# Kernel tuning notes

Hardware: AMD Instinct MI355X
Metric: run time of the kernel (lower is better)

Reference implementation:

```python
import jax, jax.numpy as jnp
import numpy as np

CUTOFF = 4.0
RBF_N = 32          # distance_embedding_size == D_rbf
F_DIM = 128         # hidden_size
N_ATOMS = 20000
N_PROBES = 100000
N_EDGES = 262144
LN_EPS = 1e-5


def setup_inputs() -> dict:
    key = jax.random.key(0)
    ks = jax.random.split(key, 20)
    s = 0.02
    inp = {
        "diff_pi": jax.random.normal(ks[0], (N_EDGES, 3), jnp.float32),
        "S_JK": jax.random.normal(ks[1], (N_ATOMS, F_DIM), jnp.float32),
        "V_JK": jax.random.normal(ks[2], (N_ATOMS, 3, F_DIM), jnp.float32),
        "atom_idx": jax.random.randint(ks[3], (N_EDGES,), 0, N_ATOMS),
        "probe_idx": jax.random.randint(ks[4], (N_EDGES,), 0, N_PROBES),
        "num_probes": N_PROBES,
        # state branch params
        "w_s1": jax.random.normal(ks[5], (3 * F_DIM, F_DIM), jnp.float32) * s,
        "b_s1": jnp.zeros((F_DIM,), jnp.float32),
        "g_ln": jnp.ones((F_DIM,), jnp.float32),
        "b_ln": jnp.zeros((F_DIM,), jnp.float32),
        "w_s2": jax.random.normal(ks[6], (F_DIM, F_DIM), jnp.float32) * s,
        "b_s2": jnp.zeros((F_DIM,), jnp.float32),
        # filter branch params
        "w_f1": jax.random.normal(ks[7], (RBF_N, F_DIM), jnp.float32) * s,
        "b_f1": jnp.zeros((F_DIM,), jnp.float32),
        "w_f2": jax.random.normal(ks[8], (F_DIM, F_DIM), jnp.float32) * s,
        "b_f2": jnp.zeros((F_DIM,), jnp.float32),
        # output head params
        "w_o1": jax.random.normal(ks[9], (F_DIM, F_DIM // 2), jnp.float32) * s,
        "b_o1": jnp.zeros((F_DIM // 2,), jnp.float32),
        "w_o2": jax.random.normal(ks[10], (F_DIM // 2, 1), jnp.float32) * s,
        "b_o2": jnp.zeros((1,), jnp.float32),
        "final_bias": jnp.array([-6.1], jnp.float32),
    }
    return inp


def reference(diff_pi, S_JK, V_JK, atom_idx, probe_idx, num_probes,
              w_s1, b_s1, g_ln, b_ln, w_s2, b_s2,
              w_f1, b_f1, w_f2, b_f2,
              w_o1, b_o1, w_o2, b_o2, final_bias):
    silu = jax.nn.silu
    # edge distances
    sq = (diff_pi ** 2).sum(-1)                       # [E]
    dist = jnp.sqrt(sq)                               # [E] exact distance
    dist_safe = jnp.sqrt(sq + 1e-8)[:, None]          # [E,1]
    r_hat = diff_pi / dist_safe                       # [E,3]

    # sinc RBF expansion: sin(n*pi*d/cutoff)/d, n=1..RBF_N
    n = jnp.arange(1, RBF_N + 1, dtype=diff_pi.dtype) # [D]
    e_pi = jnp.sin(dist[:, None] * n * (jnp.pi / CUTOFF)) / dist[:, None]  # [E,D]

    # gather atom features to edges
    n_i = jnp.sqrt((V_JK ** 2).sum(1) + 1e-8)         # [N,F]
    n_e = n_i[atom_idx]                               # [E,F]
    V_e = V_JK[atom_idx]                              # [E,3,F]
    q_pi = (V_e * r_hat[:, :, None]).sum(1)           # [E,F]
    S_e = S_JK[atom_idx]                              # [E,F]

    # state branch: Linear -> LayerNorm -> SiLU -> Linear
    h = jnp.concatenate([S_e, n_e, q_pi], axis=-1)    # [E,3F]
    u = h @ w_s1 + b_s1                               # [E,F]
    mu = u.mean(-1, keepdims=True)
    var = ((u - mu) ** 2).mean(-1, keepdims=True)
    u_norm = (u - mu) / jnp.sqrt(var + LN_EPS) * g_ln + b_ln
    state = silu(u_norm) @ w_s2 + b_s2                # [E,F]

    # filter branch (no normalization -> absolute distance scale)
    W = silu(e_pi @ w_f1 + b_f1) @ w_f2 + b_f2        # [E,F]

    # fuse + output head
    m = (silu((W * state) @ w_o1 + b_o1) @ w_o2 + b_o2)[:, 0]  # [E]

    x = dist / CUTOFF
    env = 1.0 - 21.0 * x ** 5 + 35.0 * x ** 6 - 15.0 * x ** 7
    env = jnp.where(dist < CUTOFF, env, jnp.zeros_like(env))
    m_w = m * env

    # scatter-add to probes
    rho = jax.ops.segment_sum(m_w, probe_idx, num_segments=num_probes)
    return rho + final_bias[0]
```

## Files before the change

### kernel.cpp

```cpp
#include <hip/hip_runtime.h>

#define EPB     64
#define E_TOTAL 262144
#define NPROBE  100000
#define N_ATOMS 20000

#define ASTR   136
#define A2_O   0
#define F1_O   8704
#define EPI_O  17408
#define LDS_SH 19968

#define WS1_O  0
#define WS2_O  49152
#define WF1_O  65536
#define WF2_O  69632
#define WO1_O  86016
#define WT_TOT 94208
#define PQ_O   WT_TOT

typedef __attribute__((ext_vector_type(8))) short          short8;
typedef __attribute__((ext_vector_type(8))) unsigned short ushort8;
typedef __attribute__((ext_vector_type(4))) float          floatx4;

#define MFMA16(a, b, c) __builtin_amdgcn_mfma_f32_16x16x32_bf16((a), (b), (c), 0, 0, 0)

__device__ __forceinline__ short f2bf(float x) {
    unsigned u = __builtin_bit_cast(unsigned, x);
    u = (u + 0x7FFFu + ((u >> 16) & 1u)) >> 16;
    return (short)(unsigned short)u;
}
__device__ __forceinline__ unsigned pk2(float lo, float hi) {
    return __builtin_amdgcn_perm(__builtin_bit_cast(unsigned, hi),
                                 __builtin_bit_cast(unsigned, lo), 0x07060302u);
}
__device__ __forceinline__ float bf2f(unsigned short u) {
    return __builtin_bit_cast(float, ((unsigned)u) << 16);
}
__device__ __forceinline__ float silu_f(float x) {
    return x * __builtin_amdgcn_rcpf(1.0f + __expf(-x));
}

struct F8 { float v[8]; };
__device__ __forceinline__ F8 ld8(const float* __restrict__ p) {
    F8 r;
    const float4 a = *(const float4*)p;
    const float4 b = *(const float4*)(p + 4);
    r.v[0] = a.x; r.v[1] = a.y; r.v[2] = a.z; r.v[3] = a.w;
    r.v[4] = b.x; r.v[5] = b.y; r.v[6] = b.z; r.v[7] = b.w;
    return r;
}

__global__ void cfr_prep_w(const float* __restrict__ w_s1, const float* __restrict__ w_s2,
                           const float* __restrict__ w_f1, const float* __restrict__ w_f2,
                           const float* __restrict__ w_o1,
                           const float* __restrict__ fb, float* __restrict__ out,
                           unsigned short* __restrict__ wt) {
    int i = blockIdx.x * 256 + threadIdx.x;
    if (i < NPROBE) out[i] = fb[0];
    if (i < WT_TOT) {
        float v;
        if (i < WS2_O)      { int n = i / 384, k = i - n * 384;          v = w_s1[k * 128 + n]; }
        else if (i < WF1_O) { int j = i - WS2_O, n = j >> 7, k = j & 127; v = w_s2[k * 128 + n]; }
        else if (i < WF2_O) { int j = i - WF1_O, n = j >> 5, k = j & 31;  v = w_f1[k * 128 + n]; }
        else if (i < WO1_O) { int j = i - WF2_O, n = j >> 7, k = j & 127; v = w_f2[k * 128 + n]; }
        else                { int j = i - WO1_O, n = j >> 7, k = j & 127; v = w_o1[k * 64 + n]; }
        wt[i] = (unsigned short)f2bf(v);
    }
}

__global__ __launch_bounds__(256, 2) void cfr_prep_pq(
    const float* __restrict__ S, const float* __restrict__ V,
    const float* __restrict__ b_s1,
    const unsigned short* __restrict__ wt, unsigned short* __restrict__ pq)
{
    __shared__ __align__(16) unsigned short bufH[64 * 256];
    __shared__ __align__(16) unsigned short bufV[192 * 128];

    const int t    = threadIdx.x;
    const int a0   = blockIdx.x * 64;
    const int wave = t >> 6;
    const int lane = t & 63;
    const int q    = lane >> 4;
    const int c16  = lane & 15;

#pragma unroll
    for (int it = 0; it < 4; ++it) {
        int idx = it * 256 + t;
        int al = idx >> 4, f8 = (idx & 15) * 8;
        int a = a0 + al;
        ushort8 sS, sN, s0, s1, s2;
        if (a < N_ATOMS) {
            F8 s  = ld8(S + a * 128 + f8);
            F8 v0 = ld8(V + a * 384 + f8);
            F8 v1 = ld8(V + a * 384 + 128 + f8);
            F8 v2 = ld8(V + a * 384 + 256 + f8);
#pragma unroll
            for (int j = 0; j < 8; ++j) {
                sS[j] = (unsigned short)f2bf(s.v[j]);
                sN[j] = (unsigned short)f2bf(sqrtf(v0.v[j]*v0.v[j] + v1.v[j]*v1.v[j] + v2.v[j]*v2.v[j] + 1e-8f));
                s0[j] = (unsigned short)f2bf(v0.v[j]);
                s1[j] = (unsigned short)f2bf(v1.v[j]);
                s2[j] = (unsigned short)f2bf(v2.v[j]);
            }
        } else {
#pragma unroll
            for (int j = 0; j < 8; ++j) { sS[j]=0; sN[j]=0; s0[j]=0; s1[j]=0; s2[j]=0; }
        }
        const unsigned swH = (unsigned)((al & 7) << 4);
        char* hrow  = (char*)bufH + al * 512;
        char* vbase = (char*)bufV;
        *(ushort8*)(hrow + ((f8 * 2) ^ swH))         = sS;
        *(ushort8*)(hrow + ((256 + f8 * 2) ^ swH))   = sN;
        *(ushort8*)(vbase + al * 256         + ((f8 * 2) ^ swH)) = s0;
        *(ushort8*)(vbase + (64 + al) * 256  + ((f8 * 2) ^ swH)) = s1;
        *(ushort8*)(vbase + (128 + al) * 256 + ((f8 * 2) ^ swH)) = s2;
    }
    __syncthreads();

    const floatx4 zero4 = {0.f, 0.f, 0.f, 0.f};
    const unsigned swr = (unsigned)((c16 & 7) << 4);
    float bs1c[2];
#pragma unroll
    for (int ni = 0; ni < 2; ++ni) bs1c[ni] = b_s1[wave * 32 + ni * 16 + c16];

    {
        floatx4 pacc[4][2];
#pragma unroll
        for (int mi = 0; mi < 4; ++mi) { pacc[mi][0] = zero4; pacc[mi][1] = zero4; }
#pragma unroll
        for (int kk = 0; kk < 8; ++kk) {
            short8 bfr[2], af[4];
#pragma unroll
            for (int ni = 0; ni < 2; ++ni) {
                int n = wave * 32 + ni * 16 + c16;
                bfr[ni] = *(const short8*)&wt[WS1_O + n * 384 + kk * 32 + q * 8];
            }
#pragma unroll
            for (int mi = 0; mi < 4; ++mi) {
                int row = mi * 16 + c16;
                af[mi] = *(const short8*)((const char*)bufH + row * 512 + ((unsigned)(kk * 64 + q * 16) ^ swr));
            }
#pragma unroll
            for (int mi = 0; mi < 4; ++mi)
#pragma unroll
                for (int ni = 0; ni < 2; ++ni)
                    pacc[mi][ni] = MFMA16(af[mi], bfr[ni], pacc[mi][ni]);
        }
#pragma unroll
        for (int mi = 0; mi < 4; ++mi)
#pragma unroll
            for (int r = 0; r < 4; ++r) {
                int a = a0 + mi * 16 + q * 4 + r;
                if (a < N_ATOMS)
#pragma unroll
                    for (int ni = 0; ni < 2; ++ni) {
                        int col = wave * 32 + ni * 16 + c16;
                        pq[a * 512 + col] = (unsigned short)f2bf(pacc[mi][ni][r] + bs1c[ni]);
                    }
            }
    }

    short8 bq[4][2];
#pragma unroll
    for (int kk = 0; kk < 4; ++kk)
#pragma unroll
        for (int ni = 0; ni < 2; ++ni) {
            int n = wave * 32 + ni * 16 + c16;
            bq[kk][ni] = *(const short8*)&wt[WS1_O + n * 384 + 256 + kk * 32 + q * 8];
        }
#pragma unroll
    for (int d = 0; d < 3; ++d) {
        floatx4 qacc[4][2];
#pragma unroll
        for (int mi = 0; mi < 4; ++mi) { qacc[mi][0] = zero4; qacc[mi][1] = zero4; }
#pragma unroll
        for (int kk = 0; kk < 4; ++kk) {
            short8 af[4];
#pragma unroll
            for (int mi = 0; mi < 4; ++mi) {
                int row = d * 64 + mi * 16 + c16;
                af[mi] = *(const short8*)((const char*)bufV + row * 256 + ((unsigned)(kk * 64 + q * 16) ^ swr));
            }
#pragma unroll
            for (int mi = 0; mi < 4; ++mi)
#pragma unroll
                for (int ni = 0; ni < 2; ++ni)
                    qacc[mi][ni] = MFMA16(af[mi], bq[kk][ni], qacc[mi][ni]);
        }
#pragma unroll
        for (int mi = 0; mi < 4; ++mi)
#pragma unroll
            for (int r = 0; r < 4; ++r) {
                int a = a0 + mi * 16 + q * 4 + r;
                if (a < N_ATOMS)
#pragma unroll
                    for (int ni = 0; ni < 2; ++ni) {
                        int col = wave * 32 + ni * 16 + c16;
                        pq[a * 512 + (1 + d) * 128 + col] = (unsigned short)f2bf(qacc[mi][ni][r]);
                    }
            }
    }
}

__global__ __launch_bounds__(256, 4) void cfr_main(
    const float* __restrict__ diff,
    const int* __restrict__ atom_idx, const int* __restrict__ probe_idx,
    const unsigned short* __restrict__ wt, const unsigned short* __restrict__ pq,
    const float* __restrict__ g_ln, const float* __restrict__ b_ln,
    const float* __restrict__ b_s2, const float* __restrict__ b_f1,
    const float* __restrict__ b_f2, const float* __restrict__ b_o1,
    const float* __restrict__ w_o2, const float* __restrict__ b_o2,
    float* __restrict__ out)
{
    __shared__ __align__(16) unsigned short LDSu[LDS_SH];
    float* mpart = (float*)&LDSu[EPI_O];

    const int t    = threadIdx.x;
    const int e0   = blockIdx.x * EPB;
    const int wave = t >> 6;
    const int lane = t & 63;
    const int q    = lane >> 4;
    const int c16  = lane & 15;
    const floatx4 zero4 = {0.f, 0.f, 0.f, 0.f};

    {
        const int el = t >> 2;
        const int c0 = (t & 3) * 32;
        const int eg = e0 + el;
        const int a  = atom_idx[eg];
        float dx = diff[eg * 3 + 0], dy = diff[eg * 3 + 1], dz = diff[eg * 3 + 2];
        float sq   = dx * dx + dy * dy + dz * dz;
        float dist = sqrtf(sq);
        float rinv = rsqrtf(sq + 1e-8f);
        float rx = dx * rinv, ry = dy * rinv, rz = dz * rinv;

        const ushort8* pqr = (const ushort8*)(pq + a * 512 + c0);
        float u[32];
#pragma unroll
        for (int g = 0; g < 4; ++g) {
            ushort8 v = pqr[g];
#pragma unroll
            for (int j = 0; j < 8; ++j) u[g * 8 + j] = bf2f(v[j]);
        }
#pragma unroll
        for (int g = 0; g < 4; ++g) {
            ushort8 v = pqr[16 + g];
#pragma unroll
            for (int j = 0; j < 8; ++j) u[g * 8 + j] = fmaf(bf2f(v[j]), rx, u[g * 8 + j]);
        }
#pragma unroll
        for (int g = 0; g < 4; ++g) {
            ushort8 v = pqr[32 + g];
#pragma unroll
            for (int j = 0; j < 8; ++j) u[g * 8 + j] = fmaf(bf2f(v[j]), ry, u[g * 8 + j]);
        }
#pragma unroll
        for (int g = 0; g < 4; ++g) {
            ushort8 v = pqr[48 + g];
#pragma unroll
            for (int j = 0; j < 8; ++j) u[g * 8 + j] = fmaf(bf2f(v[j]), rz, u[g * 8 + j]);
        }
        float s = 0.f, s2 = 0.f;
#pragma unroll
        for (int j = 0; j < 32; ++j) { s += u[j]; s2 = fmaf(u[j], u[j], s2); }
        s  += __shfl_xor(s, 1);  s  += __shfl_xor(s, 2);
        s2 += __shfl_xor(s2, 1); s2 += __shfl_xor(s2, 2);
        float mu = s * (1.f / 128.f);
        float rstd = rsqrtf(s2 * (1.f / 128.f) - mu * mu + 1e-5f);
        const float4* gp = (const float4*)(g_ln + c0);
        const float4* bp = (const float4*)(b_ln + c0);
        unsigned pko[16];
#pragma unroll
        for (int g4 = 0; g4 < 8; ++g4) {
            float4 gg = gp[g4], bb = bp[g4];
            float y0 = silu_f((u[g4 * 4 + 0] - mu) * rstd * gg.x + bb.x);
            float y1 = silu_f((u[g4 * 4 + 1] - mu) * rstd * gg.y + bb.y);
            float y2 = silu_f((u[g4 * 4 + 2] - mu) * rstd * gg.z + bb.z);
            float y3 = silu_f((u[g4 * 4 + 3] - mu) * rstd * gg.w + bb.w);
            pko[g4 * 2 + 0] = pk2(y0, y1);
            pko[g4 * 2 + 1] = pk2(y2, y3);
        }
        uint4* dst = (uint4*)&LDSu[A2_O + el * ASTR + c0];
        dst[0] = make_uint4(pko[0], pko[1], pko[2], pko[3]);
        dst[1] = make_uint4(pko[4], pko[5], pko[6], pko[7]);
        dst[2] = make_uint4(pko[8], pko[9], pko[10], pko[11]);
        dst[3] = make_uint4(pko[12], pko[13], pko[14], pko[15]);
        float inv = __builtin_amdgcn_rcpf(dist);
        float d8  = dist * 0.125f;
        float sv[8];
#pragma unroll
        for (int j = 0; j < 8; ++j) {
            float nf = (float)((t & 3) * 8 + j + 1);
            sv[j] = __builtin_amdgcn_sinf(d8 * nf) * inv;
        }
        *(uint4*)&LDSu[EPI_O + el * 40 + (t & 3) * 8] =
            make_uint4(pk2(sv[0], sv[1]), pk2(sv[2], sv[3]), pk2(sv[4], sv[5]), pk2(sv[6], sv[7]));
    }
    __syncthreads();

    {
        short8 ae[4], be[2];
#pragma unroll
        for (int mi = 0; mi < 4; ++mi)
            ae[mi] = *(const short8*)&LDSu[EPI_O + (mi * 16 + c16) * 40 + q * 8];
#pragma unroll
        for (int ni = 0; ni < 2; ++ni) {
            int n = wave * 32 + ni * 16 + c16;
            be[ni] = *(const short8*)&wt[WF1_O + n * 32 + q * 8];
        }
        floatx4 facc[4][2];
#pragma unroll
        for (int mi = 0; mi < 4; ++mi)
#pragma unroll
            for (int ni = 0; ni < 2; ++ni)
                facc[mi][ni] = MFMA16(ae[mi], be[ni], zero4);
        float bf1c[2];
#pragma unroll
        for (int ni = 0; ni < 2; ++ni) bf1c[ni] = b_f1[wave * 32 + ni * 16 + c16];
#pragma unroll
        for (int mi = 0; mi < 4; ++mi)
#pragma unroll
            for (int r = 0; r < 4; ++r) {
                int row = mi * 16 + q * 4 + r;
#pragma unroll
                for (int ni = 0; ni < 2; ++ni) {
                    float v = facc[mi][ni][r] + bf1c[ni];
                    LDSu[F1_O + row * ASTR + (wave * 32 + ni * 16 + c16)] =
                        (unsigned short)(__builtin_bit_cast(unsigned, silu_f(v)) >> 16);
                }
            }
    }
    __syncthreads();

    {
        floatx4 sacc[4][2], wacc[4][2];
#pragma unroll
        for (int mi = 0; mi < 4; ++mi)
#pragma unroll
            for (int ni = 0; ni < 2; ++ni) { sacc[mi][ni] = zero4; wacc[mi][ni] = zero4; }
#pragma unroll
        for (int kk = 0; kk < 4; ++kk) {
            short8 a2f[4], f1f[4], b2[2], bw[2];
#pragma unroll
            for (int ni = 0; ni < 2; ++ni) {
                int n = wave * 32 + ni * 16 + c16;
                b2[ni] = *(const short8*)&wt[WS2_O + n * 128 + kk * 32 + q * 8];
                bw[ni] = *(const short8*)&wt[WF2_O + n * 128 + kk * 32 + q * 8];
            }
#pragma unroll
            for (int mi = 0; mi < 4; ++mi) {
                a2f[mi] = *(const short8*)&LDSu[A2_O + (mi * 16 + c16) * ASTR + kk * 32 + q * 8];
                f1f[mi] = *(const short8*)&LDSu[F1_O + (mi * 16 + c16) * ASTR + kk * 32 + q * 8];
            }
#pragma unroll
            for (int mi = 0; mi < 4; ++mi)
#pragma unroll
                for (int ni = 0; ni < 2; ++ni) {
                    sacc[mi][ni] = MFMA16(a2f[mi], b2[ni], sacc[mi][ni]);
                    wacc[mi][ni] = MFMA16(f1f[mi], bw[ni], wacc[mi][ni]);
                }
        }
        __syncthreads();
        float bs2c[2], bf2c[2];
#pragma unroll
        for (int ni = 0; ni < 2; ++ni) {
            int col = wave * 32 + ni * 16 + c16;
            bs2c[ni] = b_s2[col]; bf2c[ni] = b_f2[col];
        }
#pragma unroll
        for (int mi = 0; mi < 4; ++mi)
#pragma unroll
            for (int r = 0; r < 4; ++r) {
                int row = mi * 16 + q * 4 + r;
#pragma unroll
                for (int ni = 0; ni < 2; ++ni) {
                    float g = (sacc[mi][ni][r] + bs2c[ni]) * (wacc[mi][ni][r] + bf2c[ni]);
                    LDSu[A2_O + row * ASTR + (wave * 32 + ni * 16 + c16)] =
                        (unsigned short)(__builtin_bit_cast(unsigned, g) >> 16);
                }
            }
    }
    __syncthreads();

    {
        const int n2 = wave * 16 + c16;
        floatx4 oacc[4];
#pragma unroll
        for (int mi = 0; mi < 4; ++mi) oacc[mi] = zero4;
#pragma unroll
        for (int kk = 0; kk < 4; ++kk) {
            short8 bfr = *(const short8*)&wt[WO1_O + n2 * 128 + kk * 32 + q * 8];
#pragma unroll
            for (int mi = 0; mi < 4; ++mi) {
                short8 af = *(const short8*)&LDSu[A2_O + (mi * 16 + c16) * ASTR + kk * 32 + q * 8];
                oacc[mi] = MFMA16(af, bfr, oacc[mi]);
            }
        }
        float bo1c = b_o1[n2], wo2c = w_o2[n2];
#pragma unroll
        for (int mi = 0; mi < 4; ++mi)
#pragma unroll
            for (int r = 0; r < 4; ++r) {
                float s = silu_f(oacc[mi][r] + bo1c) * wo2c;
#pragma unroll
                for (int d = 1; d < 16; d <<= 1) s += __shfl_xor(s, d, 64);
                if (c16 == 0) mpart[(mi * 16 + q * 4 + r) * 4 + wave] = s;
            }
    }
    __syncthreads();

    if (t < EPB) {
        int eg = e0 + t;
        float m = mpart[t * 4 + 0] + mpart[t * 4 + 1] + mpart[t * 4 + 2] + mpart[t * 4 + 3] + b_o2[0];
        float dx = diff[eg * 3 + 0], dy = diff[eg * 3 + 1], dz = diff[eg * 3 + 2];
        float dist = sqrtf(dx * dx + dy * dy + dz * dz);
        float x  = dist * 0.25f;
        float x2 = x * x, x4 = x2 * x2;
        float x5 = x4 * x, x6 = x5 * x, x7 = x6 * x;
        float env = 1.0f - 21.0f * x5 + 35.0f * x6 - 15.0f * x7;
        env = (dist < 4.0f) ? env : 0.0f;
        float mw = m * env;
        if (mw != 0.f) unsafeAtomicAdd(&out[probe_idx[eg]], mw);
    }
}

extern "C" void kernel_launch(void* const* d_in, const int* in_sizes, int n_in,
                              void* d_out, int out_size, void* d_ws, size_t ws_size,
                              hipStream_t stream) {
    const float* diff    = (const float*)d_in[0];
    const float* S_JK    = (const float*)d_in[1];
    const float* V_JK    = (const float*)d_in[2];
    const int*   atom_i  = (const int*)d_in[3];
    const int*   probe_i = (const int*)d_in[4];
    const float* w_s1 = (const float*)d_in[6];
    const float* b_s1 = (const float*)d_in[7];
    const float* g_ln = (const float*)d_in[8];
    const float* b_ln = (const float*)d_in[9];
    const float* w_s2 = (const float*)d_in[10];
    const float* b_s2 = (const float*)d_in[11];
    const float* w_f1 = (const float*)d_in[12];
    const float* b_f1 = (const float*)d_in[13];
    const float* w_f2 = (const float*)d_in[14];
    const float* b_f2 = (const float*)d_in[15];
    const float* w_o1 = (const float*)d_in[16];
    const float* b_o1 = (const float*)d_in[17];
    const float* w_o2 = (const float*)d_in[18];
    const float* b_o2 = (const float*)d_in[19];
    const float* fbias = (const float*)d_in[20];
    float* out = (float*)d_out;

    unsigned short* wt = (unsigned short*)d_ws;
    unsigned short* pqp = wt + PQ_O;

    cfr_prep_w<<<(NPROBE + 255) / 256, 256, 0, stream>>>(w_s1, w_s2, w_f1, w_f2, w_o1,
                                                         fbias, out, wt);
    cfr_prep_pq<<<(N_ATOMS + 63) / 64, 256, 0, stream>>>(S_JK, V_JK, b_s1, wt, pqp);
    cfr_main<<<E_TOTAL / EPB, 256, 0, stream>>>(diff, atom_i, probe_i, wt, pqp,
        g_ln, b_ln, b_s2, b_f1, b_f2, b_o1, w_o2, b_o2, out);
}
```

Measured before the change: 232.1 us.

## Halve edges per block to 32 with two-wave blocks and wider per-wave tiles

The main kernel now handles 32 edges per block with 128 threads (2 waves) instead of 64 edges with 256 threads. Each wave covers 64 output columns instead of 32 in the MLP GEMMs, and the output head uses two column tiles per wave. The per-edge distance is cached in LDS so the final envelope step no longer reloads diff. The aim is smaller LDS use per block and more resident blocks, at the cost of more weight fragment loads per edge and more registers per wave.

```diff
diff --git a/kernel.cpp b/kernel.cpp
--- a/kernel.cpp
+++ b/kernel.cpp
@@ -1,15 +1,17 @@
 #include <hip/hip_runtime.h>
 
-#define EPB     64
+#define EPB     32
+#define THREADS 128
 #define E_TOTAL 262144
 #define NPROBE  100000
 #define N_ATOMS 20000
 
 #define ASTR   136
 #define A2_O   0
-#define F1_O   8704
-#define EPI_O  17408
-#define LDS_SH 19968
+#define F1_O   4352
+#define EPI_O  8704
+#define DIST_O 9984
+#define LDS_SH 10048
 
 #define WS1_O  0
 #define WS2_O  49152
@@ -203,7 +205,7 @@
     }
 }
 
-__global__ __launch_bounds__(256, 4) void cfr_main(
+__global__ __launch_bounds__(THREADS, 4) void cfr_main(
     const float* __restrict__ diff,
     const int* __restrict__ atom_idx, const int* __restrict__ probe_idx,
     const unsigned short* __restrict__ wt, const unsigned short* __restrict__ pq,
@@ -215,6 +217,7 @@
 {
     __shared__ __align__(16) unsigned short LDSu[LDS_SH];
     float* mpart = (float*)&LDSu[EPI_O];
+    float* distL = (float*)&LDSu[DIST_O];
 
     const int t    = threadIdx.x;
     const int e0   = blockIdx.x * EPB;
@@ -226,7 +229,8 @@
 
     {
         const int el = t >> 2;
-        const int c0 = (t & 3) * 32;
+        const int cc = t & 3;
+        const int c0 = cc * 32;
         const int eg = e0 + el;
         const int a  = atom_idx[eg];
         float dx = diff[eg * 3 + 0], dy = diff[eg * 3 + 1], dz = diff[eg * 3 + 2];
@@ -234,6 +238,7 @@
         float dist = sqrtf(sq);
         float rinv = rsqrtf(sq + 1e-8f);
         float rx = dx * rinv, ry = dy * rinv, rz = dz * rinv;
+        if (cc == 0) distL[el] = dist;
 
         const ushort8* pqr = (const ushort8*)(pq + a * 512 + c0);
         float u[32];
@@ -291,42 +296,42 @@
         float sv[8];
 #pragma unroll
         for (int j = 0; j < 8; ++j) {
-            float nf = (float)((t & 3) * 8 + j + 1);
+            float nf = (float)(cc * 8 + j + 1);
             sv[j] = __builtin_amdgcn_sinf(d8 * nf) * inv;
         }
-        *(uint4*)&LDSu[EPI_O + el * 40 + (t & 3) * 8] =
+        *(uint4*)&LDSu[EPI_O + el * 40 + cc * 8] =
             make_uint4(pk2(sv[0], sv[1]), pk2(sv[2], sv[3]), pk2(sv[4], sv[5]), pk2(sv[6], sv[7]));
     }
     __syncthreads();
 
     {
-        short8 ae[4], be[2];
-#pragma unroll
-        for (int mi = 0; mi < 4; ++mi)
+        short8 ae[2], be[4];
+#pragma unroll
+        for (int mi = 0; mi < 2; ++mi)
             ae[mi] = *(const short8*)&LDSu[EPI_O + (mi * 16 + c16) * 40 + q * 8];
 #pragma unroll
-        for (int ni = 0; ni < 2; ++ni) {
-            int n = wave * 32 + ni * 16 + c16;
+        for (int ni = 0; ni < 4; ++ni) {
+            int n = wave * 64 + ni * 16 + c16;
             be[ni] = *(const short8*)&wt[WF1_O + n * 32 + q * 8];
         }
-        floatx4 facc[4][2];
-#pragma unroll
-        for (int mi = 0; mi < 4; ++mi)
-#pragma unroll
-            for (int ni = 0; ni < 2; ++ni)
+        floatx4 facc[2][4];
+#pragma unroll
+        for (int mi = 0; mi < 2; ++mi)
+#pragma unroll
+            for (int ni = 0; ni < 4; ++ni)
                 facc[mi][ni] = MFMA16(ae[mi], be[ni], zero4);
-        float bf1c[2];
-#pragma unroll
-        for (int ni = 0; ni < 2; ++ni) bf1c[ni] = b_f1[wave * 32 + ni * 16 + c16];
-#pragma unroll
-        for (int mi = 0; mi < 4; ++mi)
+        float bf1c[4];
+#pragma unroll
+        for (int ni = 0; ni < 4; ++ni) bf1c[ni] = b_f1[wave * 64 + ni * 16 + c16];
+#pragma unroll
+        for (int mi = 0; mi < 2; ++mi)
 #pragma unroll
             for (int r = 0; r < 4; ++r) {
                 int row = mi * 16 + q * 4 + r;
 #pragma unroll
-                for (int ni = 0; ni < 2; ++ni) {
+                for (int ni = 0; ni < 4; ++ni) {
                     float v = facc[mi][ni][r] + bf1c[ni];
-                    LDSu[F1_O + row * ASTR + (wave * 32 + ni * 16 + c16)] =
+                    LDSu[F1_O + row * ASTR + (wave * 64 + ni * 16 + c16)] =
                         (unsigned short)(__builtin_bit_cast(unsigned, silu_f(v)) >> 16);
                 }
             }
@@ -334,49 +339,49 @@
     __syncthreads();
 
     {
-        floatx4 sacc[4][2], wacc[4][2];
-#pragma unroll
-        for (int mi = 0; mi < 4; ++mi)
-#pragma unroll
-            for (int ni = 0; ni < 2; ++ni) { sacc[mi][ni] = zero4; wacc[mi][ni] = zero4; }
+        floatx4 sacc[2][4], wacc[2][4];
+#pragma unroll
+        for (int mi = 0; mi < 2; ++mi)
+#pragma unroll
+            for (int ni = 0; ni < 4; ++ni) { sacc[mi][ni] = zero4; wacc[mi][ni] = zero4; }
 #pragma unroll
         for (int kk = 0; kk < 4; ++kk) {
-            short8 a2f[4], f1f[4], b2[2], bw[2];
-#pragma unroll
-            for (int ni = 0; ni < 2; ++ni) {
-                int n = wave * 32 + ni * 16 + c16;
+            short8 a2f[2], f1f[2], b2[4], bw[4];
+#pragma unroll
+            for (int ni = 0; ni < 4; ++ni) {
+                int n = wave * 64 + ni * 16 + c16;
                 b2[ni] = *(const short8*)&wt[WS2_O + n * 128 + kk * 32 + q * 8];
                 bw[ni] = *(const short8*)&wt[WF2_O + n * 128 + kk * 32 + q * 8];
             }
 #pragma unroll
-            for (int mi = 0; mi < 4; ++mi) {
+            for (int mi = 0; mi < 2; ++mi) {
                 a2f[mi] = *(const short8*)&LDSu[A2_O + (mi * 16 + c16) * ASTR + kk * 32 + q * 8];
                 f1f[mi] = *(const short8*)&LDSu[F1_O + (mi * 16 + c16) * ASTR + kk * 32 + q * 8];
             }
 #pragma unroll
-            for (int mi = 0; mi < 4; ++mi)
-#pragma unroll
-                for (int ni = 0; ni < 2; ++ni) {
+            for (int mi = 0; mi < 2; ++mi)
+#pragma unroll
+                for (int ni = 0; ni < 4; ++ni) {
                     sacc[mi][ni] = MFMA16(a2f[mi], b2[ni], sacc[mi][ni]);
                     wacc[mi][ni] = MFMA16(f1f[mi], bw[ni], wacc[mi][ni]);
                 }
         }
         __syncthreads();
-        float bs2c[2], bf2c[2];
-#pragma unroll
-        for (int ni = 0; ni < 2; ++ni) {
-            int col = wave * 32 + ni * 16 + c16;
+        float bs2c[4], bf2c[4];
+#pragma unroll
+        for (int ni = 0; ni < 4; ++ni) {
+            int col = wave * 64 + ni * 16 + c16;
             bs2c[ni] = b_s2[col]; bf2c[ni] = b_f2[col];
         }
 #pragma unroll
-        for (int mi = 0; mi < 4; ++mi)
+        for (int mi = 0; mi < 2; ++mi)
 #pragma unroll
             for (int r = 0; r < 4; ++r) {
                 int row = mi * 16 + q * 4 + r;
 #pragma unroll
-                for (int ni = 0; ni < 2; ++ni) {
+                for (int ni = 0; ni < 4; ++ni) {
                     float g = (sacc[mi][ni][r] + bs2c[ni]) * (wacc[mi][ni][r] + bf2c[ni]);
-                    LDSu[A2_O + row * ASTR + (wave * 32 + ni * 16 + c16)] =
+                    LDSu[A2_O + row * ASTR + (wave * 64 + ni * 16 + c16)] =
                         (unsigned short)(__builtin_bit_cast(unsigned, g) >> 16);
                 }
             }
@@ -384,37 +389,48 @@
     __syncthreads();
 
     {
-        const int n2 = wave * 16 + c16;
-        floatx4 oacc[4];
-#pragma unroll
-        for (int mi = 0; mi < 4; ++mi) oacc[mi] = zero4;
+        floatx4 oacc[2][2];
+#pragma unroll
+        for (int mi = 0; mi < 2; ++mi) { oacc[mi][0] = zero4; oacc[mi][1] = zero4; }
 #pragma unroll
         for (int kk = 0; kk < 4; ++kk) {
-            short8 bfr = *(const short8*)&wt[WO1_O + n2 * 128 + kk * 32 + q * 8];
-#pragma unroll
-            for (int mi = 0; mi < 4; ++mi) {
+            short8 bfr[2];
+#pragma unroll
+            for (int ni = 0; ni < 2; ++ni) {
+                int n2 = wave * 32 + ni * 16 + c16;
+                bfr[ni] = *(const short8*)&wt[WO1_O + n2 * 128 + kk * 32 + q * 8];
+            }
+#pragma unroll
+            for (int mi = 0; mi < 2; ++mi) {
                 short8 af = *(const short8*)&LDSu[A2_O + (mi * 16 + c16) * ASTR + kk * 32 + q * 8];
-                oacc[mi] = MFMA16(af, bfr, oacc[mi]);
-            }
-        }
-        float bo1c = b_o1[n2], wo2c = w_o2[n2];
-#pragma unroll
-        for (int mi = 0; mi < 4; ++mi)
+#pragma unroll
+                for (int ni = 0; ni < 2; ++ni)
+                    oacc[mi][ni] = MFMA16(af, bfr[ni], oacc[mi][ni]);
+            }
+        }
+        float bo1c[2], wo2c[2];
+#pragma unroll
+        for (int ni = 0; ni < 2; ++ni) {
+            int n2 = wave * 32 + ni * 16 + c16;
+            bo1c[ni] = b_o1[n2]; wo2c[ni] = w_o2[n2];
+        }
+#pragma unroll
+        for (int mi = 0; mi < 2; ++mi)
 #pragma unroll
             for (int r = 0; r < 4; ++r) {
-                float s = silu_f(oacc[mi][r] + bo1c) * wo2c;
+                float s = silu_f(oacc[mi][0][r] + bo1c[0]) * wo2c[0]
+                        + silu_f(oacc[mi][1][r] + bo1c[1]) * wo2c[1];
 #pragma unroll
                 for (int d = 1; d < 16; d <<= 1) s += __shfl_xor(s, d, 64);
-                if (c16 == 0) mpart[(mi * 16 + q * 4 + r) * 4 + wave] = s;
+                if (c16 == 0) mpart[(mi * 16 + q * 4 + r) * 2 + wave] = s;
             }
     }
     __syncthreads();
 
     if (t < EPB) {
         int eg = e0 + t;
-        float m = mpart[t * 4 + 0] + mpart[t * 4 + 1] + mpart[t * 4 + 2] + mpart[t * 4 + 3] + b_o2[0];
-        float dx = diff[eg * 3 + 0], dy = diff[eg * 3 + 1], dz = diff[eg * 3 + 2];
-        float dist = sqrtf(dx * dx + dy * dy + dz * dz);
+        float m = mpart[t * 2 + 0] + mpart[t * 2 + 1] + b_o2[0];
+        float dist = distL[t];
         float x  = dist * 0.25f;
         float x2 = x * x, x4 = x2 * x2;
         float x5 = x4 * x, x6 = x5 * x, x7 = x6 * x;
@@ -456,6 +472,6 @@
     cfr_prep_w<<<(NPROBE + 255) / 256, 256, 0, stream>>>(w_s1, w_s2, w_f1, w_f2, w_o1,
                                                          fbias, out, wt);
     cfr_prep_pq<<<(N_ATOMS + 63) / 64, 256, 0, stream>>>(S_JK, V_JK, b_s1, wt, pqp);
-    cfr_main<<<E_TOTAL / EPB, 256, 0, stream>>>(diff, atom_i, probe_i, wt, pqp,
+    cfr_main<<<E_TOTAL / EPB, THREADS, 0, stream>>>(diff, atom_i, probe_i, wt, pqp,
         g_ln, b_ln, b_s2, b_f1, b_f2, b_o1, w_o2, b_o2, out);
 }
```

Result: slower. 265.9 us (+14.6%).

## Counting-sort edges by atom index before main kernel to improve gather locality

Applied to the files above, without the earlier changes.

Adds histogram, single-block scan, and scatter kernels that reorder edges (atom index, probe index, diff vectors) by atom, then runs the main kernel on the sorted arrays. The aim is to make the per-edge gathers of precomputed per-atom data hit cache more often, since consecutive edges now share atoms. It costs three extra launches, atomics, a serial single-block scan, and extra workspace traffic, and it only activates when the workspace is large enough. Probe scatter atomics become less coalesced, because probe order is now arbitrary within each atom's group.

```diff
diff --git a/kernel.cpp b/kernel.cpp
--- a/kernel.cpp
+++ b/kernel.cpp
@@ -18,6 +18,12 @@
 #define WO1_O  86016
 #define WT_TOT 94208
 #define PQ_O   WT_TOT
+#define CNT_B    20668416u
+#define OFF_B    20748416u
+#define ATOMS_B  20828416u
+#define PROBES_B 21876992u
+#define DIFFS_B  22925568u
+#define WS_NEED  26071296u
 
 typedef __attribute__((ext_vector_type(8))) short          short8;
 typedef __attribute__((ext_vector_type(8))) unsigned short ushort8;
@@ -55,9 +61,10 @@
                            const float* __restrict__ w_f1, const float* __restrict__ w_f2,
                            const float* __restrict__ w_o1,
                            const float* __restrict__ fb, float* __restrict__ out,
-                           unsigned short* __restrict__ wt) {
+                           unsigned short* __restrict__ wt, int* __restrict__ cnt) {
     int i = blockIdx.x * 256 + threadIdx.x;
     if (i < NPROBE) out[i] = fb[0];
+    if (cnt && i < N_ATOMS) cnt[i] = 0;
     if (i < WT_TOT) {
         float v;
         if (i < WS2_O)      { int n = i / 384, k = i - n * 384;          v = w_s1[k * 128 + n]; }
@@ -66,6 +73,43 @@
         else if (i < WO1_O) { int j = i - WF2_O, n = j >> 7, k = j & 127; v = w_f2[k * 128 + n]; }
         else                { int j = i - WO1_O, n = j >> 7, k = j & 127; v = w_o1[k * 64 + n]; }
         wt[i] = (unsigned short)f2bf(v);
+    }
+}
+
+__global__ void cfr_hist(const int* __restrict__ atom_idx, int* __restrict__ cnt) {
+    int e = blockIdx.x * 256 + threadIdx.x;
+    if (e < E_TOTAL) atomicAdd(&cnt[atom_idx[e]], 1);
+}
+
+__global__ void cfr_scan(const int* __restrict__ cnt, int* __restrict__ off) {
+    __shared__ int part[256], base[256];
+    const int t  = threadIdx.x;
+    const int CH = (N_ATOMS + 255) / 256;
+    int lo = t * CH, hi = lo + CH; if (hi > N_ATOMS) hi = N_ATOMS;
+    int s = 0;
+    for (int i = lo; i < hi; ++i) s += cnt[i];
+    part[t] = s;
+    __syncthreads();
+    if (t == 0) { int acc = 0; for (int i = 0; i < 256; ++i) { base[i] = acc; acc += part[i]; } }
+    __syncthreads();
+    int acc = base[t];
+    for (int i = lo; i < hi; ++i) { off[i] = acc; acc += cnt[i]; }
+}
+
+__global__ void cfr_scatter(const float* __restrict__ diff, const int* __restrict__ atom_idx,
+                            const int* __restrict__ probe_idx, int* __restrict__ off,
+                            int* __restrict__ atom_s, int* __restrict__ probe_s,
+                            float* __restrict__ diff_s) {
+    int e = blockIdx.x * 256 + threadIdx.x;
+    if (e < E_TOTAL) {
+        int a   = atom_idx[e];
+        int pos = atomicAdd(&off[a], 1);
+        atom_s[pos]  = a;
+        probe_s[pos] = probe_idx[e];
+        float d0 = diff[e * 3 + 0], d1 = diff[e * 3 + 1], d2 = diff[e * 3 + 2];
+        diff_s[pos * 3 + 0] = d0;
+        diff_s[pos * 3 + 1] = d1;
+        diff_s[pos * 3 + 2] = d2;
     }
 }
 
@@ -450,12 +494,30 @@
     const float* fbias = (const float*)d_in[20];
     float* out = (float*)d_out;
 
-    unsigned short* wt = (unsigned short*)d_ws;
+    char* wsb = (char*)d_ws;
+    unsigned short* wt  = (unsigned short*)wsb;
     unsigned short* pqp = wt + PQ_O;
 
+    const bool use_sort = (ws_size >= (size_t)WS_NEED);
+    int*   cnt     = use_sort ? (int*)(wsb + CNT_B)    : (int*)nullptr;
+    int*   offp    = (int*)(wsb + OFF_B);
+    int*   atom_s  = (int*)(wsb + ATOMS_B);
+    int*   probe_s = (int*)(wsb + PROBES_B);
+    float* diff_s  = (float*)(wsb + DIFFS_B);
+
     cfr_prep_w<<<(NPROBE + 255) / 256, 256, 0, stream>>>(w_s1, w_s2, w_f1, w_f2, w_o1,
-                                                         fbias, out, wt);
+                                                         fbias, out, wt, cnt);
     cfr_prep_pq<<<(N_ATOMS + 63) / 64, 256, 0, stream>>>(S_JK, V_JK, b_s1, wt, pqp);
-    cfr_main<<<E_TOTAL / EPB, 256, 0, stream>>>(diff, atom_i, probe_i, wt, pqp,
-        g_ln, b_ln, b_s2, b_f1, b_f2, b_o1, w_o2, b_o2, out);
-}
+
+    if (use_sort) {
+        cfr_hist<<<E_TOTAL / 256, 256, 0, stream>>>(atom_i, cnt);
+        cfr_scan<<<1, 256, 0, stream>>>(cnt, offp);
+        cfr_scatter<<<E_TOTAL / 256, 256, 0, stream>>>(diff, atom_i, probe_i, offp,
+                                                       atom_s, probe_s, diff_s);
+        cfr_main<<<E_TOTAL / EPB, 256, 0, stream>>>(diff_s, atom_s, probe_s, wt, pqp,
+            g_ln, b_ln, b_s2, b_f1, b_f2, b_o1, w_o2, b_o2, out);
+    } else {
+        cfr_main<<<E_TOTAL / EPB, 256, 0, stream>>>(diff, atom_i, probe_i, wt, pqp,
+            g_ln, b_ln, b_s2, b_f1, b_f2, b_o1, w_o2, b_o2, out);
+    }
+}
```

New measurement: 299.2 us. 1.29x slower.
